# Kernel optimization log

Measured on AMD Instinct MI355X. Metric: run time of the kernel, lower is better.

## Reference

```python
import jax, jax.numpy as jnp
from jax import lax
import numpy as np

# pywt db4 filter bank (ascending order)
DEC_LO = np.array([-0.010597401784997278, 0.032883011666982945, 0.030841381835986965,
                   -0.18703481171888114, -0.02798376941698385, 0.6308807679295904,
                   0.7148465705525415, 0.23037781330885523], dtype=np.float32)
F_LEN = DEC_LO.shape[0]
_signs = ((-1.0) ** (np.arange(F_LEN) + 1)).astype(np.float32)
DEC_HI = _signs * DEC_LO[::-1]
REC_LO = DEC_LO[::-1].copy()
REC_HI = DEC_HI[::-1].copy()
# conv filters flipped -> cross-correlation kernels for lax.conv
DEC_K = np.stack([DEC_LO[::-1], DEC_HI[::-1]])[:, None, :]   # (2, 1, F): lo/hi analysis
REC_K = np.stack([REC_LO[::-1], REC_HI[::-1]])[None, :, :]   # (1, 2, F): synthesis, sums lo+hi
LEVELS = 3


def dwt_level(x, dec_k):
    """One symmetric-mode DWT level. x: (M, n) -> (cA, cD) each (M, floor((n+F-1)/2))."""
    f = dec_k.shape[-1]
    x_ext = jnp.pad(x, ((0, 0), (f - 1, f - 1)), mode='symmetric')[:, 1:]
    y = lax.conv_general_dilated(x_ext[:, None, :], dec_k, (2,), 'VALID',
                                 dimension_numbers=('NCH', 'OIH', 'NCH'))
    return y[:, 0], y[:, 1]


def idwt_level(ca, cd, rec_k, out_len):
    """One IDWT level; trims to out_len (original length at that level)."""
    f = rec_k.shape[-1]
    m, L = ca.shape
    up = jnp.zeros((m, 2, 2 * L), ca.dtype).at[:, 0, ::2].set(ca).at[:, 1, ::2].set(cd)
    y = lax.conv_general_dilated(up, rec_k, (1,), [(f - 1, f - 1)],
                                 dimension_numbers=('NCH', 'OIH', 'NCH'))[:, 0]
    s = f - 2
    return y[:, s:s + out_len]


def setup_inputs() -> dict:
    key = jax.random.key(0)
    B, N, D = 8, 4096, 768
    x = jax.random.normal(key, (B, N, D), dtype=jnp.float32)
    w_approx = jnp.ones((D,), dtype=jnp.float32)
    w_details = jnp.ones((LEVELS, D), dtype=jnp.float32)
    return {"x": x, "w_approx": w_approx, "w_details": w_details}


def reference(x, w_approx, w_details):
    B, N, D = x.shape
    dec_k = jnp.asarray(DEC_K)
    rec_k = jnp.asarray(REC_K)
    # all channels processed at once: (B, N, D) -> (B*D, N)
    sig = x.transpose(0, 2, 1).reshape(B * D, N)
    # J-level decomposition, recording per-level lengths for reconstruction
    a = sig
    lengths = []
    details = []
    for _ in range(LEVELS):
        lengths.append(a.shape[-1])
        a, d = dwt_level(a, dec_k)
        details.append(d)
    # pointwise mixing: one scalar per channel per band (matches ones(1,1,D) param sliced per-channel)
    def chan(w):  # (D,) -> (B*D, 1)
        return jnp.broadcast_to(w, (B, D)).reshape(B * D, 1)
    a = a * chan(w_approx)
    details = [d * chan(w_details[j]) for j, d in enumerate(details)]
    # reconstruction
    rec = a
    for j in reversed(range(LEVELS)):
        rec = idwt_level(rec, details[j], rec_k, lengths[j])
    rec = rec.reshape(B, D, N).transpose(0, 2, 1)
    # residual connection (dropout=0.0)
    return x + rec
```

## Files before the change

### kernel.cpp

```cpp
#include <hip/hip_runtime.h>


namespace {

constexpr int NT  = 256;
constexpr int N0  = 4096;
constexpr int DCH = 768;
constexpr int TS  = 128;
constexpr int TE  = 256;
constexpr int G   = 8;
constexpr int NDG = DCH / G;
constexpr int L1v = 2051, L2v = 1029, L3v = 518;

constexpr int NSEG = (N0 - 2 * TE) / TS;
constexpr int NINT = 8 * 3 * NSEG;

constexpr int SP = 972;
constexpr int OX = 0, OA1 = 356, OD1 = 536, OA2 = 716, OD2 = 804,
              OA3 = 892, OD3 = 932, OREC = 716;

__device__ constexpr float LO[8] = {
  -0.010597401784997278f,  0.032883011666982945f,  0.030841381835986965f,
  -0.18703481171888114f,  -0.02798376941698385f,   0.6308807679295904f,
   0.7148465705525415f,    0.23037781330885523f };
__device__ constexpr float HI[8] = {
  -0.23037781330885523f,   0.7148465705525415f,   -0.6308807679295904f,
  -0.02798376941698385f,   0.18703481171888114f,   0.030841381835986965f,
  -0.032883011666982945f, -0.010597401784997278f };
__device__ constexpr float LOF[8] = {
   0.23037781330885523f,   0.7148465705525415f,    0.6308807679295904f,
  -0.02798376941698385f,  -0.18703481171888114f,   0.030841381835986965f,
   0.032883011666982945f, -0.010597401784997278f };
__device__ constexpr float HIF[8] = {
  -0.010597401784997278f, -0.032883011666982945f,  0.030841381835986965f,
   0.18703481171888114f,  -0.02798376941698385f,  -0.6308807679295904f,
   0.7148465705525415f,   -0.23037781330885523f };

__device__ __forceinline__ int refl(int g, int n) {
  g = (g < 0) ? (-g - 1) : g;
  return (g >= n) ? (2 * n - 1 - g) : g;
}

struct Streams {
  float xa[22];
  float a1a[14], d1a[29];
  float a2a[10], d2a[13];
  float a3a[5],  d3a[5];
  float r2a[7],  r1a[11];
};

template <int SMODE>
__device__ __forceinline__ void superstep(Streams& S,
                                          const float* __restrict__ xrow,
                                          float* __restrict__ orow, int bk8,
                                          float wa, float w0, float w1,
                                          float w2) {
#pragma unroll
  for (int i = 0; i < 16; ++i)
    S.xa[6 + i] = xrow[(long)(bk8 - 48 + i) * DCH];

  float rres[16];
  if (SMODE != 0) {
#pragma unroll
    for (int i = 0; i < 16; ++i)
      rres[i] = xrow[(long)(bk8 - 90 + i) * DCH];
  }

#pragma unroll
  for (int u = 0; u < 2; ++u) {
#pragma unroll
    for (int j = 0; j < 4; ++j) {
      float slo = 0.f, shi = 0.f;
#pragma unroll
      for (int k = 0; k < 8; ++k) {
        const float v = S.xa[8 * u + 2 * j + k];
        slo = fmaf(LOF[k], v, slo);
        shi = fmaf(HIF[k], v, shi);
      }
      S.a1a[6 + 4 * u + j]  = slo;
      S.d1a[21 + 4 * u + j] = w0 * shi;
    }
#pragma unroll
    for (int i = 0; i < 2; ++i) {
      float slo = 0.f, shi = 0.f;
#pragma unroll
      for (int k = 0; k < 8; ++k) {
        const float v = S.a1a[4 * u + 2 * i + k];
        slo = fmaf(LOF[k], v, slo);
        shi = fmaf(HIF[k], v, shi);
      }
      S.a2a[6 + 2 * u + i] = slo;
      S.d2a[9 + 2 * u + i] = w1 * shi;
    }
    {
      float slo = 0.f, shi = 0.f;
#pragma unroll
      for (int k = 0; k < 8; ++k) {
        const float v = S.a2a[2 * u + k];
        slo = fmaf(LOF[k], v, slo);
        shi = fmaf(HIF[k], v, shi);
      }
      S.a3a[3 + u] = wa * slo;
      S.d3a[3 + u] = w2 * shi;
    }
    {
      float e = 0.f, o = 0.f;
#pragma unroll
      for (int m = 0; m < 4; ++m) {
        e = fmaf(LO[2 * m + 1], S.a3a[u + m], e);
        e = fmaf(HI[2 * m + 1], S.d3a[u + m], e);
        o = fmaf(LO[2 * m],     S.a3a[u + m], o);
        o = fmaf(HI[2 * m],     S.d3a[u + m], o);
      }
      S.r2a[3 + 2 * u]     = e;
      S.r2a[3 + 2 * u + 1] = o;
    }
#pragma unroll
    for (int h = 0; h < 2; ++h) {
      float e = 0.f, o = 0.f;
#pragma unroll
      for (int m = 0; m < 4; ++m) {
        e = fmaf(LO[2 * m + 1], S.r2a[2 * u + h + m], e);
        e = fmaf(HI[2 * m + 1], S.d2a[2 * u + h + m], e);
        o = fmaf(LO[2 * m],     S.r2a[2 * u + h + m], o);
        o = fmaf(HI[2 * m],     S.d2a[2 * u + h + m], o);
      }
      S.r1a[3 + 4 * u + 2 * h]     = e;
      S.r1a[3 + 4 * u + 2 * h + 1] = o;
    }
    if (SMODE != 0) {
#pragma unroll
      for (int tau = 0; tau < 4; ++tau) {
        bool doSt;
        if (SMODE == 2)      doSt = true;
        else if (SMODE == 1) doSt = (u == 1) && (tau >= 1);
        else                 doSt = (u == 0) || (tau == 0);
        if (doSt) {
          float e = 0.f, o = 0.f;
#pragma unroll
          for (int m = 0; m < 4; ++m) {
            e = fmaf(LO[2 * m + 1], S.r1a[4 * u + tau + m], e);
            e = fmaf(HI[2 * m + 1], S.d1a[4 * u + tau + m], e);
            o = fmaf(LO[2 * m],     S.r1a[4 * u + tau + m], o);
            o = fmaf(HI[2 * m],     S.d1a[4 * u + tau + m], o);
          }
          const long ofs = bk8 + 8 * u - 90 + 2 * tau;
          orow[ofs * DCH]       = e + rres[8 * u + 2 * tau];
          orow[(ofs + 1) * DCH] = o + rres[8 * u + 2 * tau + 1];
        }
      }
    }
  }
#pragma unroll
  for (int i = 0; i < 6; ++i)  S.xa[i]  = S.xa[i + 16];
#pragma unroll
  for (int i = 0; i < 6; ++i)  S.a1a[i] = S.a1a[i + 8];
#pragma unroll
  for (int i = 0; i < 21; ++i) S.d1a[i] = S.d1a[i + 8];
#pragma unroll
  for (int i = 0; i < 6; ++i)  S.a2a[i] = S.a2a[i + 4];
#pragma unroll
  for (int i = 0; i < 9; ++i)  S.d2a[i] = S.d2a[i + 4];
#pragma unroll
  for (int i = 0; i < 3; ++i) { S.a3a[i] = S.a3a[i + 2]; S.d3a[i] = S.d3a[i + 2]; }
#pragma unroll
  for (int i = 0; i < 3; ++i)  S.r2a[i] = S.r2a[i + 4];
#pragma unroll
  for (int i = 0; i < 3; ++i)  S.r1a[i] = S.r1a[i + 8];
}


__device__ void analyze_g(const float* __restrict__ in, int Oin,
                          float* __restrict__ oa, float* __restrict__ od,
                          int cnt, int Oout, int lenout, int i2) {
  for (int p = i2; p < cnt; p += 32) {
    const int gp = refl(Oout + p, lenout);
    const int qb = 2 * gp - 6 - Oin;
    float alo = 0.f, ahi = 0.f;
#pragma unroll
    for (int k = 0; k < 8; ++k) {
      const float v = in[qb + k];
      alo = fmaf(LOF[k], v, alo);
      ahi = fmaf(HIF[k], v, ahi);
    }
    oa[p] = alo;
    od[p] = ahi;
  }
}

__device__ void synth_g(const float* __restrict__ ca,
                        const float* __restrict__ cd, int doff,
                        float* __restrict__ o, float sa, float sd, int npair,
                        int i2) {
  for (int t = i2; t < npair; t += 32) {
    float e = 0.f, ed = 0.f, oe = 0.f, od_ = 0.f;
#pragma unroll
    for (int m = 0; m < 4; ++m) {
      e   = fmaf(LO[2 * m + 1], ca[t + m], e);
      ed  = fmaf(HI[2 * m + 1], cd[t + doff + m], ed);
      oe  = fmaf(LO[2 * m],     ca[t + m], oe);
      od_ = fmaf(HI[2 * m],     cd[t + doff + m], od_);
    }
    o[2 * t]     = sa * e  + sd * ed;
    o[2 * t + 1] = sa * oe + sd * od_;
  }
}

}

__global__ __launch_bounds__(NT) void wavemix_kernel(
    const float* __restrict__ x, const float* __restrict__ wap,
    const float* __restrict__ wdet, float* __restrict__ out) {
  __shared__ float pool[G * SP];
  const int blk = blockIdx.x;
  const int tid = threadIdx.x;

  if (blk < NINT) {
    const int wgs    = (blk & 7) * (NINT >> 3) + (blk >> 3);
    const int si     = wgs % NSEG;
    const int row    = wgs / NSEG;
    const int wgroup = row % 3;
    const int b      = row / 3;
    const int n0     = (si + 2) * TS;
    const int d      = wgroup * 256 + tid;

    const float* __restrict__ xrow = x   + ((size_t)b * N0 + n0) * DCH + d;
    float* __restrict__       orow = out + ((size_t)b * N0 + n0) * DCH + d;
    const float wa = wap[d];
    const float w0 = wdet[d];
    const float w1 = wdet[DCH + d];
    const float w2 = wdet[2 * DCH + d];

    Streams S = {};
    int bk8 = 0;
#pragma unroll 1
    for (int m = 0; m < 5; ++m) {
      superstep<0>(S, xrow, orow, bk8, wa, w0, w1, w2);
      bk8 += 16;
    }
    superstep<1>(S, xrow, orow, bk8, wa, w0, w1, w2);
    bk8 += 16;
#pragma unroll 1
    for (int m = 0; m < 7; ++m) {
      superstep<2>(S, xrow, orow, bk8, wa, w0, w1, w2);
      bk8 += 16;
    }
    superstep<3>(S, xrow, orow, bk8, wa, w0, w1, w2);
  } else {
    const int e    = blk - NINT;
    const int nt   = (e & 1) ? 15 : 0;
    const int rest = e >> 1;
    const int dg   = rest % NDG;
    const int b    = rest / NDG;
    const int n0   = nt * TE;
    const int d0   = dg * G;

    {
      const int q  = tid & 1;
      const int pl = tid >> 1;
      for (int p = pl; p < 352; p += 128) {
        const int g = refl(n0 - 46 + p, N0);
        const float4 v = *reinterpret_cast<const float4*>(
            x + ((size_t)b * N0 + g) * DCH + d0 + 4 * q);
        float* dst = pool + (4 * q) * SP + OX + p;
        dst[0]      = v.x;
        dst[SP]     = v.y;
        dst[2 * SP] = v.z;
        dst[3 * SP] = v.w;
      }
    }

    const int c2 = tid >> 5;
    const int i2 = tid & 31;
    float* P = pool + c2 * SP;
    const float wa = wap[d0 + c2];
    const float w2 = wdet[2 * DCH + d0 + c2];
    const float w1 = wdet[1 * DCH + d0 + c2];
    const float w0 = wdet[0 * DCH + d0 + c2];
    __syncthreads();

    analyze_g(P + OX,  n0 - 46,     P + OA1, P + OD1, 172, n0 / 2 - 20, L1v, i2);
    __syncthreads();
    analyze_g(P + OA1, n0 / 2 - 20, P + OA2, P + OD2,  82, n0 / 4 - 6,  L2v, i2);
    __syncthreads();
    analyze_g(P + OA2, n0 / 4 - 6,  P + OA3, P + OD3,  38, n0 / 8,      L3v, i2);
    __syncthreads();
    synth_g(P + OA3, P + OD3, 0, P + OA2, wa,  w2, 35, i2);
    __syncthreads();
    synth_g(P + OA2, P + OD2, 6, P + OA1, 1.f, w1, 66, i2);
    __syncthreads();
    for (int t = i2; t < 128; t += 32) {
      const float* pa = P + OA1;
      const float* pd = P + OD1;
      float e2 = 0.f, ed = 0.f, oe = 0.f, od_ = 0.f;
#pragma unroll
      for (int m = 0; m < 4; ++m) {
        e2  = fmaf(LO[2 * m + 1], pa[t + m], e2);
        ed  = fmaf(HI[2 * m + 1], pd[t + 20 + m], ed);
        oe  = fmaf(LO[2 * m],     pa[t + m], oe);
        od_ = fmaf(HI[2 * m],     pd[t + 20 + m], od_);
      }
      (P + OREC)[2 * t]     = e2 + w0 * ed  + (P + OX)[2 * t + 46];
      (P + OREC)[2 * t + 1] = oe + w0 * od_ + (P + OX)[2 * t + 47];
    }
    __syncthreads();

    {
      const int c = tid & 7;
      const int j = tid >> 3;
      const float* R = pool + c * SP + OREC;
      float* orow = out + ((size_t)b * N0 + n0) * DCH + d0 + c;
      for (int pos = j; pos < TE; pos += 32)
        orow[(size_t)pos * DCH] = R[pos];
    }
  }
}

extern "C" void kernel_launch(void* const* d_in, const int* in_sizes, int n_in,
                              void* d_out, int out_size, void* d_ws, size_t ws_size,
                              hipStream_t stream) {
  const float* x  = (const float*)d_in[0];
  const float* wa = (const float*)d_in[1];
  const float* wd = (const float*)d_in[2];
  float* out      = (float*)d_out;

  const int grid = NINT + 8 * NDG * 2;
  wavemix_kernel<<<grid, NT, 0, stream>>>(x, wa, wd, out);
}
```

Baseline: 64.32 us.

## Software-pipeline global loads one superstep ahead and shrink interior segment size

Splits each superstep into a load-issue phase and a compute phase, using double-buffered register arrays so the next 16 input rows and residual rows are fetched while the current step computes. The interior loop is restructured into an explicitly unrolled prologue plus a 2x-unrolled steady-state loop. The segment size drops from 128 to 112 and interior tiles now start at TE, which changes the number of interior blocks and their coverage. This hides global-load latency at the cost of more live registers, which may reduce occupancy.

```diff
diff --git a/kernel.cpp b/kernel.cpp
--- a/kernel.cpp
+++ b/kernel.cpp
@@ -6,7 +6,7 @@
 constexpr int NT  = 256;
 constexpr int N0  = 4096;
 constexpr int DCH = 768;
-constexpr int TS  = 128;
+constexpr int TS  = 112;
 constexpr int TE  = 256;
 constexpr int G   = 8;
 constexpr int NDG = DCH / G;
@@ -49,22 +49,30 @@
   float r2a[7],  r1a[11];
 };
 
+__device__ __forceinline__ void issue_stream(float (&L)[16],
+                                             const float* __restrict__ xrow,
+                                             int bk8) {
+  const float* __restrict__ p = xrow + (long)(bk8 - 48) * DCH;
+#pragma unroll
+  for (int i = 0; i < 16; ++i) L[i] = p[(size_t)i * DCH];
+}
+
+__device__ __forceinline__ void issue_res(float (&R)[16],
+                                          const float* __restrict__ xrow,
+                                          int bk8) {
+  const float* __restrict__ p = xrow + (long)(bk8 - 90) * DCH;
+#pragma unroll
+  for (int i = 0; i < 16; ++i) R[i] = p[(size_t)i * DCH];
+}
+
 template <int SMODE>
-__device__ __forceinline__ void superstep(Streams& S,
-                                          const float* __restrict__ xrow,
-                                          float* __restrict__ orow, int bk8,
-                                          float wa, float w0, float w1,
-                                          float w2) {
-#pragma unroll
-  for (int i = 0; i < 16; ++i)
-    S.xa[6 + i] = xrow[(long)(bk8 - 48 + i) * DCH];
-
-  float rres[16];
-  if (SMODE != 0) {
-#pragma unroll
-    for (int i = 0; i < 16; ++i)
-      rres[i] = xrow[(long)(bk8 - 90 + i) * DCH];
-  }
+__device__ __forceinline__ void compute_step(Streams& S, const float (&L)[16],
+                                             const float (&R)[16],
+                                             float* __restrict__ orow, int bk8,
+                                             float wa, float w0, float w1,
+                                             float w2) {
+#pragma unroll
+  for (int i = 0; i < 16; ++i) S.xa[6 + i] = L[i];
 
 #pragma unroll
   for (int u = 0; u < 2; ++u) {
@@ -145,8 +153,8 @@
             o = fmaf(HI[2 * m],     S.d1a[4 * u + tau + m], o);
           }
           const long ofs = bk8 + 8 * u - 90 + 2 * tau;
-          orow[ofs * DCH]       = e + rres[8 * u + 2 * tau];
-          orow[(ofs + 1) * DCH] = o + rres[8 * u + 2 * tau + 1];
+          orow[ofs * DCH]       = e + R[8 * u + 2 * tau];
+          orow[(ofs + 1) * DCH] = o + R[8 * u + 2 * tau + 1];
         }
       }
     }
@@ -221,7 +229,7 @@
     const int row    = wgs / NSEG;
     const int wgroup = row % 3;
     const int b      = row / 3;
-    const int n0     = (si + 2) * TS;
+    const int n0     = TE + si * TS;
     const int d      = wgroup * 256 + tid;
 
     const float* __restrict__ xrow = x   + ((size_t)b * N0 + n0) * DCH + d;
@@ -232,20 +240,30 @@
     const float w2 = wdet[2 * DCH + d];
 
     Streams S = {};
-    int bk8 = 0;
+    float LA[16], LB[16], RA[16], RB[16];
+
+    issue_stream(LA, xrow, 0);
+    issue_stream(LB, xrow, 16);
+    compute_step<0>(S, LA, RA, orow, 0,  wa, w0, w1, w2);
+    issue_stream(LA, xrow, 32);
+    compute_step<0>(S, LB, RA, orow, 16, wa, w0, w1, w2);
+    issue_stream(LB, xrow, 48);
+    compute_step<0>(S, LA, RA, orow, 32, wa, w0, w1, w2);
+    issue_stream(LA, xrow, 64);
+    compute_step<0>(S, LB, RA, orow, 48, wa, w0, w1, w2);
+    issue_stream(LB, xrow, 80); issue_res(RA, xrow, 80);
+    compute_step<0>(S, LA, RA, orow, 64, wa, w0, w1, w2);
+    issue_stream(LA, xrow, 96); issue_res(RB, xrow, 96);
+    compute_step<1>(S, LB, RA, orow, 80, wa, w0, w1, w2);
 #pragma unroll 1
-    for (int m = 0; m < 5; ++m) {
-      superstep<0>(S, xrow, orow, bk8, wa, w0, w1, w2);
-      bk8 += 16;
-    }
-    superstep<1>(S, xrow, orow, bk8, wa, w0, w1, w2);
-    bk8 += 16;
-#pragma unroll 1
-    for (int m = 0; m < 7; ++m) {
-      superstep<2>(S, xrow, orow, bk8, wa, w0, w1, w2);
-      bk8 += 16;
-    }
-    superstep<3>(S, xrow, orow, bk8, wa, w0, w1, w2);
+    for (int m = 0; m < 3; ++m) {
+      const int b0 = 96 + 32 * m;
+      issue_stream(LB, xrow, b0 + 16); issue_res(RA, xrow, b0 + 16);
+      compute_step<2>(S, LA, RB, orow, b0,      wa, w0, w1, w2);
+      issue_stream(LA, xrow, b0 + 32); issue_res(RB, xrow, b0 + 32);
+      compute_step<2>(S, LB, RA, orow, b0 + 16, wa, w0, w1, w2);
+    }
+    compute_step<3>(S, LA, RB, orow, 192, wa, w0, w1, w2);
   } else {
     const int e    = blk - NINT;
     const int nt   = (e & 1) ? 15 : 0;
```

Result: slower. 69.28 us (+7.7%).
